# Kernel tuning notes

Hardware: AMD Instinct MI355X
Metric: run time of the kernel (lower is better)

## Reference

```python
import jax, jax.numpy as jnp
import numpy as np

N_NODES = 50000
N_EDGES = 1600000
IN_DIM = 6
H = 64


def _sage_conv(x, src, dst, W_l, b_l, W_r, num_nodes):
    """PyG SAGEConv (aggr='mean'): out = lin_l(mean_{j in N(i)} x_j) + lin_r(x_i).
    lin_l has bias, lin_r has no bias (PyG default)."""
    # mean-aggregate neighbor features at destination nodes
    agg = jax.ops.segment_sum(x[src], dst, num_segments=num_nodes)          # [N, d]
    cnt = jax.ops.segment_sum(jnp.ones((src.shape[0],), x.dtype), dst,
                              num_segments=num_nodes)                        # [N]
    mean = agg / jnp.maximum(cnt, 1.0)[:, None]
    return mean @ W_l + b_l + x @ W_r


def setup_inputs() -> dict:
    key = jax.random.key(0)
    ks = jax.random.split(key, 8)
    x = jax.random.normal(ks[0], (N_NODES, IN_DIM), dtype=jnp.float32)
    edge_index = jax.random.randint(ks[1], (2, N_EDGES), 0, N_NODES, dtype=jnp.int64)
    # Kaiming-ish scaled params
    def lin(k, fan_in, fan_out):
        return jax.random.normal(k, (fan_in, fan_out), dtype=jnp.float32) / np.sqrt(fan_in)
    return {
        "x": x,
        "edge_index": edge_index,
        "W1_l": lin(ks[2], IN_DIM, H),
        "b1_l": jnp.zeros((H,), jnp.float32),
        "W1_r": lin(ks[3], IN_DIM, H),
        "W2_l": lin(ks[4], H, H),
        "b2_l": jnp.zeros((H,), jnp.float32),
        "W2_r": lin(ks[5], H, H),
    }


def reference(x, edge_index, W1_l, b1_l, W1_r, W2_l, b2_l, W2_r):
    src, dst = edge_index[0], edge_index[1]
    n = x.shape[0]
    z = jax.nn.relu(_sage_conv(x, src, dst, W1_l, b1_l, W1_r, n))  # [N, H]
    z = _sage_conv(z, src, dst, W2_l, b2_l, W2_r, n)               # [N, H]
    return z
```

## Files before the change

kernel.cpp:

```cpp
#include <hip/hip_runtime.h>

#define N_NODES 50000
#define N_EDGES 1600000
#define IN_DIM 6
#define H 64

#define NBUCKET 196
#define NBLK 196
#define EPB 8192
#define BCAP 10240

#define L2PAD 72

__device__ __forceinline__ float bf2f(unsigned short u) {
    return __uint_as_float(((unsigned int)u) << 16);
}
__device__ __forceinline__ unsigned short f2bf(float f) {
    unsigned int u = __float_as_uint(f);
    u += 0x7fffu + ((u >> 16) & 1u);
    return (unsigned short)(u >> 16);
}

__global__ __launch_bounds__(256) void scatter_bucketed(
        const int* __restrict__ ei,
        int* __restrict__ gcur,
        unsigned int* __restrict__ ebin,
        const float* __restrict__ W2l,
        const float* __restrict__ W2r,
        unsigned short* __restrict__ Wlt,
        unsigned short* __restrict__ Wrt) {
    int t = threadIdx.x;
    if (blockIdx.x == NBLK) {
        for (int i = t; i < H * H; i += 256) {
            int k = i >> 6, f = i & 63;
            Wlt[f * H + k] = f2bf(W2l[i]);
            Wrt[f * H + k] = f2bf(W2r[i]);
        }
        return;
    }
    __shared__ unsigned int sedge[EPB];
    __shared__ int hist[NBUCKET];
    __shared__ int cur[NBUCKET];
    for (int i = t; i < NBUCKET; i += 256) hist[i] = 0;
    __syncthreads();
    int e0 = blockIdx.x * EPB;
    int cnt = min(EPB, N_EDGES - e0);
    const int4* s4 = (const int4*)(ei + e0);
    const int4* d4 = (const int4*)(ei + N_EDGES + e0);
    for (int k = t; k * 4 < cnt; k += 256) {
        int4 sv = s4[k];
        int4 dv = d4[k];
        sedge[k * 4 + 0] = ((unsigned)sv.x << 16) | (unsigned)dv.x;
        sedge[k * 4 + 1] = ((unsigned)sv.y << 16) | (unsigned)dv.y;
        sedge[k * 4 + 2] = ((unsigned)sv.z << 16) | (unsigned)dv.z;
        sedge[k * 4 + 3] = ((unsigned)sv.w << 16) | (unsigned)dv.w;
        atomicAdd(&hist[dv.x >> 8], 1);
        atomicAdd(&hist[dv.y >> 8], 1);
        atomicAdd(&hist[dv.z >> 8], 1);
        atomicAdd(&hist[dv.w >> 8], 1);
    }
    __syncthreads();
    for (int i = t; i < NBUCKET; i += 256)
        cur[i] = atomicAdd(&gcur[i], hist[i]);
    __syncthreads();
    for (int k = t; k * 4 < cnt; k += 256) {
#pragma unroll
        for (int j = 0; j < 4; j++) {
            unsigned int p = sedge[k * 4 + j];
            int b = (int)(p & 0xffffu) >> 8;
            int pos = atomicAdd(&cur[b], 1);
            if (pos < BCAP) ebin[b * BCAP + pos] = p;
        }
    }
}

__global__ __launch_bounds__(256) void bucket_build(
        const unsigned int* __restrict__ ebin,
        const int* __restrict__ gcur,
        int2* __restrict__ rowpair,
        unsigned short* __restrict__ esrc) {
    __shared__ int raw[BCAP];
    __shared__ unsigned short ssrc[BCAP];
    __shared__ int sdeg[256];
    __shared__ int scur[256];
    __shared__ int wsum[4];
    int t = threadIdx.x, lane = t & 63, w = t >> 6;
    int b = blockIdx.x;
    int base = b << 8;
    int nn = min(256, N_NODES - base);
    int ebase = b * BCAP;
    int cnt = min(gcur[b], BCAP);

    sdeg[t] = 0;
    for (int i = t; i < cnt; i += 256) raw[i] = (int)ebin[ebase + i];
    __syncthreads();
    for (int i = t; i < cnt; i += 256) atomicAdd(&sdeg[raw[i] & 0xff], 1);
    __syncthreads();
    int v = sdeg[t], s = v;
#pragma unroll
    for (int off = 1; off < 64; off <<= 1) {
        int u = __shfl_up(s, off);
        if (lane >= off) s += u;
    }
    if (lane == 63) wsum[w] = s;
    __syncthreads();
    int woff2 = 0;
    for (int k = 0; k < w; k++) woff2 += wsum[k];
    int excl = s - v + woff2;
    if (t < nn) rowpair[base + t] = make_int2(ebase + excl, ebase + excl + v);
    scur[t] = excl;
    __syncthreads();
    for (int i = t; i < cnt; i += 256) {
        int p = raw[i];
        int pos = atomicAdd(&scur[p & 0xff], 1);
        ssrc[pos] = (unsigned short)(((unsigned)p) >> 16);
    }
    __syncthreads();
    for (int i = t; i < cnt; i += 256)
        esrc[ebase + i] = ssrc[i];
}

__global__ __launch_bounds__(256) void layer1_fused(
        const float* __restrict__ x,
        const int2* __restrict__ rowpair,
        const unsigned short* __restrict__ esrc,
        const float* __restrict__ W1l,
        const float* __restrict__ b1,
        const float* __restrict__ W1r,
        unsigned short* __restrict__ z) {
    __shared__ float sWl[IN_DIM * H];
    __shared__ float sWr[IN_DIM * H];
    int t = threadIdx.x;
    for (int i = t; i < IN_DIM * H; i += 256) {
        sWl[i] = W1l[i];
        sWr[i] = W1r[i];
    }
    __syncthreads();

    int wid = t >> 6, lane = t & 63;
    int n = blockIdx.x * 4 + wid;
    if (n >= N_NODES) {
        if (t < H) z[(size_t)N_NODES * H + t] = 0;
        return;
    }
    int2 rp = rowpair[n];
    int r0 = rp.x, r1 = rp.y;
    int nh = 2 * (r1 - r0);
    int half = lane & 1;
    float a0 = 0.f, a1 = 0.f, a2 = 0.f;
    for (int hh = lane; hh < nh; hh += 64) {
        int src = esrc[r0 + (hh >> 1)];
        const float* xs = x + (size_t)src * IN_DIM + half * 3;
        a0 += xs[0]; a1 += xs[1]; a2 += xs[2];
    }
#pragma unroll
    for (int off = 2; off < 64; off <<= 1) {
        a0 += __shfl_xor(a0, off);
        a1 += __shfl_xor(a1, off);
        a2 += __shfl_xor(a2, off);
    }
    float m[IN_DIM];
    m[0] = __shfl(a0, 0); m[1] = __shfl(a1, 0); m[2] = __shfl(a2, 0);
    m[3] = __shfl(a0, 1); m[4] = __shfl(a1, 1); m[5] = __shfl(a2, 1);
    float inv = 1.0f / fmaxf((float)(r1 - r0), 1.0f);

    const float* xn = x + (size_t)n * IN_DIM;
    float acc = b1[lane];
#pragma unroll
    for (int k = 0; k < IN_DIM; k++) {
        acc += m[k] * inv * sWl[k * H + lane] + xn[k] * sWr[k * H + lane];
    }
    z[(size_t)n * H + lane] = f2bf(fmaxf(acc, 0.0f));
}

__global__ __launch_bounds__(256) void layer2_mfma(
        const unsigned short* __restrict__ zin,
        const int2* __restrict__ rowpair,
        const unsigned short* __restrict__ esrc,
        const unsigned short* __restrict__ Wlt,
        const float* __restrict__ b2,
        const unsigned short* __restrict__ Wrt,
        float* __restrict__ out) {
    typedef short bf16x8 __attribute__((ext_vector_type(8)));
    typedef float f32x4 __attribute__((ext_vector_type(4)));
    __shared__ __attribute__((aligned(16))) unsigned short smean[16 * L2PAD];
    __shared__ __attribute__((aligned(16))) unsigned short szl[16 * L2PAD];
    __shared__ __attribute__((aligned(16))) unsigned short sWl[64 * L2PAD];
    __shared__ __attribute__((aligned(16))) unsigned short sWr[64 * L2PAD];

    int t = threadIdx.x;
    int w = t >> 6, lane = t & 63;
    int g = lane >> 4, lg = lane & 15;
    int n0 = blockIdx.x * 16;

    {
        const ushort4* wl4 = (const ushort4*)Wlt;
        const ushort4* wr4 = (const ushort4*)Wrt;
        for (int qi = t; qi < H * H / 4; qi += 256) {
            int f = qi >> 4, kq = qi & 15;
            *(ushort4*)&sWl[f * L2PAD + kq * 4] = wl4[qi];
            *(ushort4*)&sWr[f * L2PAD + kq * 4] = wr4[qi];
        }
    }

    for (int q = 0; q < 4; q++) {
        int ln = w * 4 + q;
        int n = n0 + ln;
        int2 rp = rowpair[n];
        int r0 = rp.x, r1 = rp.y;
        float4 acc = make_float4(0.f, 0.f, 0.f, 0.f);
        for (int base = r0; base < r1; base += 64) {
            int ii = base + lane;
            int idx = (ii < r1) ? (int)esrc[ii] : N_NODES;
            int rem = r1 - base;
#pragma unroll 1
            for (int c = 0; c < 64; c += 16) {
                if (c >= rem) break;
#pragma unroll
                for (int tt = 0; tt < 4; tt++) {
                    int j = c + tt * 4 + g;
                    int s = __shfl(idx, j);
                    const ushort4* zr = (const ushort4*)(zin + (size_t)s * H);
                    ushort4 v = zr[lg];
                    acc.x += bf2f(v.x); acc.y += bf2f(v.y);
                    acc.z += bf2f(v.z); acc.w += bf2f(v.w);
                }
            }
        }
#pragma unroll
        for (int off = 16; off < 64; off <<= 1) {
            acc.x += __shfl_xor(acc.x, off);
            acc.y += __shfl_xor(acc.y, off);
            acc.z += __shfl_xor(acc.z, off);
            acc.w += __shfl_xor(acc.w, off);
        }
        float inv = 1.0f / fmaxf((float)(r1 - r0), 1.0f);
        if (g == 0) {
            ushort4 mb;
            mb.x = f2bf(acc.x * inv); mb.y = f2bf(acc.y * inv);
            mb.z = f2bf(acc.z * inv); mb.w = f2bf(acc.w * inv);
            *(ushort4*)&smean[ln * L2PAD + lg * 4] = mb;
        }
        szl[ln * L2PAD + lane] = zin[(size_t)n * H + lane];
    }
    __syncthreads();

    f32x4 acc = {0.f, 0.f, 0.f, 0.f};
#pragma unroll
    for (int ks = 0; ks < 2; ks++) {
        int ko = ks * 32 + g * 8;
        bf16x8 aM = *(const bf16x8*)&smean[lg * L2PAD + ko];
        bf16x8 aZ = *(const bf16x8*)&szl[lg * L2PAD + ko];
        bf16x8 bL = *(const bf16x8*)&sWl[(w * 16 + lg) * L2PAD + ko];
        bf16x8 bR = *(const bf16x8*)&sWr[(w * 16 + lg) * L2PAD + ko];
        acc = __builtin_amdgcn_mfma_f32_16x16x32_bf16(aM, bL, acc, 0, 0, 0);
        acc = __builtin_amdgcn_mfma_f32_16x16x32_bf16(aZ, bR, acc, 0, 0, 0);
    }
    float bias = b2[w * 16 + lg];
#pragma unroll
    for (int r = 0; r < 4; r++) {
        int node = n0 + g * 4 + r;
        out[(size_t)node * H + w * 16 + lg] = acc[r] + bias;
    }
}

extern "C" void kernel_launch(void* const* d_in, const int* in_sizes, int n_in,
                              void* d_out, int out_size, void* d_ws, size_t ws_size,
                              hipStream_t stream) {
    const float* x   = (const float*)d_in[0];
    const int*   ei  = (const int*)d_in[1];
    const float* W1l = (const float*)d_in[2];
    const float* b1  = (const float*)d_in[3];
    const float* W1r = (const float*)d_in[4];
    const float* W2l = (const float*)d_in[5];
    const float* b2  = (const float*)d_in[6];
    const float* W2r = (const float*)d_in[7];
    float* out = (float*)d_out;

    int* gcur = (int*)d_ws;
    int2* rowpair = (int2*)(gcur + 208);
    unsigned int*   ebin = (unsigned int*)(rowpair + N_NODES);
    unsigned short* esrc = (unsigned short*)(ebin + NBUCKET * BCAP);
    unsigned short* z    = esrc + NBUCKET * BCAP;
    unsigned short* Wlt  = z + (size_t)(N_NODES + 1) * H;
    unsigned short* Wrt  = Wlt + H * H;

    hipMemsetAsync(gcur, 0, NBUCKET * sizeof(int), stream);

    scatter_bucketed<<<NBLK + 1, 256, 0, stream>>>(ei, gcur, ebin,
                                                   W2l, W2r, Wlt, Wrt);
    bucket_build<<<NBUCKET, 256, 0, stream>>>(ebin, gcur, rowpair, esrc);

    layer1_fused<<<N_NODES / 4 + 1, 256, 0, stream>>>(x, rowpair, esrc,
                                                      W1l, b1, W1r, z);
    layer2_mfma<<<N_NODES / 16, 256, 0, stream>>>(z, rowpair, esrc,
                                                  Wlt, b2, Wrt, out);
}
```

Baseline: 161.8 us.

## Fuse CSR bucket build with layer-1 aggregation and linear in one kernel

Merges bucket_build and layer1_fused into one 512-thread kernel per 256-node bucket. Each block now reads neighbour indices from shared memory, gathers x with two threads per node, stores the means in LDS and computes the 6->64 linear layer there. This removes one kernel launch and the global round trip of esrc and rowpair before layer 1. Bucket capacity is cut to 9216, which saves memory and shared space but risks dropping edges if a bucket overflows. Layer 1 now runs on only 196 blocks, which lowers parallelism for the gather.

```diff
diff --git a/kernel.cpp b/kernel.cpp
--- a/kernel.cpp
+++ b/kernel.cpp
@@ -8,7 +8,7 @@
 #define NBUCKET 196
 #define NBLK 196
 #define EPB 8192
-#define BCAP 10240
+#define BCAP 9216
 
 #define L2PAD 72
 
@@ -28,7 +28,8 @@
         const float* __restrict__ W2l,
         const float* __restrict__ W2r,
         unsigned short* __restrict__ Wlt,
-        unsigned short* __restrict__ Wrt) {
+        unsigned short* __restrict__ Wrt,
+        unsigned short* __restrict__ z) {
     int t = threadIdx.x;
     if (blockIdx.x == NBLK) {
         for (int i = t; i < H * H; i += 256) {
@@ -36,6 +37,7 @@
             Wlt[f * H + k] = f2bf(W2l[i]);
             Wrt[f * H + k] = f2bf(W2r[i]);
         }
+        if (t < H) z[(size_t)N_NODES * H + t] = 0;
         return;
     }
     __shared__ unsigned int sedge[EPB];
@@ -69,108 +71,122 @@
             unsigned int p = sedge[k * 4 + j];
             int b = (int)(p & 0xffffu) >> 8;
             int pos = atomicAdd(&cur[b], 1);
-            if (pos < BCAP) ebin[b * BCAP + pos] = p;
-        }
-    }
-}
-
-__global__ __launch_bounds__(256) void bucket_build(
+            if (pos < BCAP) ebin[(size_t)b * BCAP + pos] = p;
+        }
+    }
+}
+
+__global__ __launch_bounds__(512) void bucket_layer1(
         const unsigned int* __restrict__ ebin,
         const int* __restrict__ gcur,
+        const float* __restrict__ x,
+        const float* __restrict__ W1l,
+        const float* __restrict__ b1,
+        const float* __restrict__ W1r,
         int2* __restrict__ rowpair,
-        unsigned short* __restrict__ esrc) {
+        unsigned short* __restrict__ esrc,
+        unsigned short* __restrict__ z) {
     __shared__ int raw[BCAP];
     __shared__ unsigned short ssrc[BCAP];
     __shared__ int sdeg[256];
+    __shared__ int sstart[256];
     __shared__ int scur[256];
     __shared__ int wsum[4];
-    int t = threadIdx.x, lane = t & 63, w = t >> 6;
+    __shared__ float sW1l[IN_DIM * H];
+    __shared__ float sW1r[IN_DIM * H];
+    float* smx   = (float*)raw;
+    float* spart = (float*)raw + 4096;
+
+    int t = threadIdx.x;
+    int lane = t & 63, w = t >> 6;
     int b = blockIdx.x;
     int base = b << 8;
     int nn = min(256, N_NODES - base);
     int ebase = b * BCAP;
     int cnt = min(gcur[b], BCAP);
 
-    sdeg[t] = 0;
-    for (int i = t; i < cnt; i += 256) raw[i] = (int)ebin[ebase + i];
-    __syncthreads();
-    for (int i = t; i < cnt; i += 256) atomicAdd(&sdeg[raw[i] & 0xff], 1);
-    __syncthreads();
-    int v = sdeg[t], s = v;
-#pragma unroll
-    for (int off = 1; off < 64; off <<= 1) {
-        int u = __shfl_up(s, off);
-        if (lane >= off) s += u;
-    }
-    if (lane == 63) wsum[w] = s;
-    __syncthreads();
-    int woff2 = 0;
-    for (int k = 0; k < w; k++) woff2 += wsum[k];
-    int excl = s - v + woff2;
-    if (t < nn) rowpair[base + t] = make_int2(ebase + excl, ebase + excl + v);
-    scur[t] = excl;
-    __syncthreads();
-    for (int i = t; i < cnt; i += 256) {
+    if (t < 256) sdeg[t] = 0;
+    for (int i = t; i < IN_DIM * H; i += 512) { sW1l[i] = W1l[i]; sW1r[i] = W1r[i]; }
+    for (int i = t; i < cnt; i += 512) raw[i] = (int)ebin[ebase + i];
+    __syncthreads();
+    for (int i = t; i < cnt; i += 512) atomicAdd(&sdeg[raw[i] & 0xff], 1);
+    __syncthreads();
+    int v = 0, s = 0;
+    if (t < 256) {
+        v = sdeg[t]; s = v;
+#pragma unroll
+        for (int off = 1; off < 64; off <<= 1) {
+            int u = __shfl_up(s, off);
+            if (lane >= off) s += u;
+        }
+        if (lane == 63) wsum[w] = s;
+    }
+    __syncthreads();
+    if (t < 256) {
+        int woff = 0;
+        for (int k = 0; k < w; k++) woff += wsum[k];
+        int excl = s - v + woff;
+        sstart[t] = excl;
+        scur[t] = excl;
+        if (t < nn) rowpair[base + t] = make_int2(ebase + excl, ebase + excl + v);
+    }
+    __syncthreads();
+    for (int i = t; i < cnt; i += 512) {
         int p = raw[i];
         int pos = atomicAdd(&scur[p & 0xff], 1);
-        ssrc[pos] = (unsigned short)(((unsigned)p) >> 16);
-    }
-    __syncthreads();
-    for (int i = t; i < cnt; i += 256)
+        ssrc[pos] = (unsigned short)((unsigned)p >> 16);
+    }
+    __syncthreads();
+    for (int i = t; i < cnt; i += 512)
         esrc[ebase + i] = ssrc[i];
-}
-
-__global__ __launch_bounds__(256) void layer1_fused(
-        const float* __restrict__ x,
-        const int2* __restrict__ rowpair,
-        const unsigned short* __restrict__ esrc,
-        const float* __restrict__ W1l,
-        const float* __restrict__ b1,
-        const float* __restrict__ W1r,
-        unsigned short* __restrict__ z) {
-    __shared__ float sWl[IN_DIM * H];
-    __shared__ float sWr[IN_DIM * H];
-    int t = threadIdx.x;
-    for (int i = t; i < IN_DIM * H; i += 256) {
-        sWl[i] = W1l[i];
-        sWr[i] = W1r[i];
-    }
-    __syncthreads();
-
-    int wid = t >> 6, lane = t & 63;
-    int n = blockIdx.x * 4 + wid;
-    if (n >= N_NODES) {
-        if (t < H) z[(size_t)N_NODES * H + t] = 0;
-        return;
-    }
-    int2 rp = rowpair[n];
-    int r0 = rp.x, r1 = rp.y;
-    int nh = 2 * (r1 - r0);
-    int half = lane & 1;
-    float a0 = 0.f, a1 = 0.f, a2 = 0.f;
-    for (int hh = lane; hh < nh; hh += 64) {
-        int src = esrc[r0 + (hh >> 1)];
-        const float* xs = x + (size_t)src * IN_DIM + half * 3;
-        a0 += xs[0]; a1 += xs[1]; a2 += xs[2];
-    }
-#pragma unroll
-    for (int off = 2; off < 64; off <<= 1) {
-        a0 += __shfl_xor(a0, off);
-        a1 += __shfl_xor(a1, off);
-        a2 += __shfl_xor(a2, off);
-    }
-    float m[IN_DIM];
-    m[0] = __shfl(a0, 0); m[1] = __shfl(a1, 0); m[2] = __shfl(a2, 0);
-    m[3] = __shfl(a0, 1); m[4] = __shfl(a1, 1); m[5] = __shfl(a2, 1);
-    float inv = 1.0f / fmaxf((float)(r1 - r0), 1.0f);
-
-    const float* xn = x + (size_t)n * IN_DIM;
-    float acc = b1[lane];
-#pragma unroll
-    for (int k = 0; k < IN_DIM; k++) {
-        acc += m[k] * inv * sWl[k * H + lane] + xn[k] * sWr[k * H + lane];
-    }
-    z[(size_t)n * H + lane] = f2bf(fmaxf(acc, 0.0f));
+    for (int i = t; i < nn * IN_DIM; i += 512) {
+        int node = i / 6, k = i - node * 6;
+        smx[node * 16 + 6 + k] = x[(size_t)base * IN_DIM + i];
+    }
+
+    int node = t & 255, half = t >> 8;
+    float a0 = 0.f, a1 = 0.f, a2 = 0.f, a3 = 0.f, a4 = 0.f, a5 = 0.f;
+    int deg = 0, st = 0;
+    if (node < nn) { deg = sdeg[node]; st = sstart[node]; }
+    for (int i = st + half; i < st + deg; i += 2) {
+        int src = ssrc[i];
+        const float2* xs = (const float2*)(x + (size_t)src * IN_DIM);
+        float2 p0 = xs[0], p1 = xs[1], p2 = xs[2];
+        a0 += p0.x; a1 += p0.y; a2 += p1.x;
+        a3 += p1.y; a4 += p2.x; a5 += p2.y;
+    }
+    if (half == 1 && node < nn) {
+        spart[node * 6 + 0] = a0; spart[node * 6 + 1] = a1;
+        spart[node * 6 + 2] = a2; spart[node * 6 + 3] = a3;
+        spart[node * 6 + 4] = a4; spart[node * 6 + 5] = a5;
+    }
+    __syncthreads();
+    if (half == 0 && node < nn) {
+        float inv = 1.0f / fmaxf((float)deg, 1.0f);
+        smx[node * 16 + 0] = (a0 + spart[node * 6 + 0]) * inv;
+        smx[node * 16 + 1] = (a1 + spart[node * 6 + 1]) * inv;
+        smx[node * 16 + 2] = (a2 + spart[node * 6 + 2]) * inv;
+        smx[node * 16 + 3] = (a3 + spart[node * 6 + 3]) * inv;
+        smx[node * 16 + 4] = (a4 + spart[node * 6 + 4]) * inv;
+        smx[node * 16 + 5] = (a5 + spart[node * 6 + 5]) * inv;
+    }
+    __syncthreads();
+
+    int feat = t & 63, ng = t >> 6;
+    float wl[IN_DIM], wr[IN_DIM];
+#pragma unroll
+    for (int k = 0; k < IN_DIM; k++) { wl[k] = sW1l[k * H + feat]; wr[k] = sW1r[k * H + feat]; }
+    float bias = b1[feat];
+    for (int nb = ng; nb < nn; nb += 8) {
+        const float4* row = (const float4*)&smx[nb * 16];
+        float4 r0 = row[0], r1 = row[1], r2 = row[2];
+        float acc = bias;
+        acc += r0.x * wl[0] + r0.y * wl[1] + r0.z * wl[2]
+             + r0.w * wl[3] + r1.x * wl[4] + r1.y * wl[5];
+        acc += r1.z * wr[0] + r1.w * wr[1] + r2.x * wr[2]
+             + r2.y * wr[3] + r2.z * wr[4] + r2.w * wr[5];
+        z[(size_t)(base + nb) * H + feat] = f2bf(fmaxf(acc, 0.0f));
+    }
 }
 
 __global__ __launch_bounds__(256) void layer2_mfma(
@@ -221,9 +237,9 @@
                     int j = c + tt * 4 + g;
                     int s = __shfl(idx, j);
                     const ushort4* zr = (const ushort4*)(zin + (size_t)s * H);
-                    ushort4 v = zr[lg];
-                    acc.x += bf2f(v.x); acc.y += bf2f(v.y);
-                    acc.z += bf2f(v.z); acc.w += bf2f(v.w);
+                    ushort4 vv = zr[lg];
+                    acc.x += bf2f(vv.x); acc.y += bf2f(vv.y);
+                    acc.z += bf2f(vv.z); acc.w += bf2f(vv.w);
                 }
             }
         }
@@ -280,19 +296,17 @@
     int* gcur = (int*)d_ws;
     int2* rowpair = (int2*)(gcur + 208);
     unsigned int*   ebin = (unsigned int*)(rowpair + N_NODES);
-    unsigned short* esrc = (unsigned short*)(ebin + NBUCKET * BCAP);
-    unsigned short* z    = esrc + NBUCKET * BCAP;
+    unsigned short* esrc = (unsigned short*)(ebin + (size_t)NBUCKET * BCAP);
+    unsigned short* z    = esrc + (size_t)NBUCKET * BCAP;
     unsigned short* Wlt  = z + (size_t)(N_NODES + 1) * H;
     unsigned short* Wrt  = Wlt + H * H;
 
     hipMemsetAsync(gcur, 0, NBUCKET * sizeof(int), stream);
 
     scatter_bucketed<<<NBLK + 1, 256, 0, stream>>>(ei, gcur, ebin,
-                                                   W2l, W2r, Wlt, Wrt);
-    bucket_build<<<NBUCKET, 256, 0, stream>>>(ebin, gcur, rowpair, esrc);
-
-    layer1_fused<<<N_NODES / 4 + 1, 256, 0, stream>>>(x, rowpair, esrc,
-                                                      W1l, b1, W1r, z);
+                                                   W2l, W2r, Wlt, Wrt, z);
+    bucket_layer1<<<NBUCKET, 512, 0, stream>>>(ebin, gcur, x, W1l, b1, W1r,
+                                               rowpair, esrc, z);
     layer2_mfma<<<N_NODES / 16, 256, 0, stream>>>(z, rowpair, esrc,
                                                   Wlt, b2, Wrt, out);
 }
```

Result: faster. 152.2 us (-5.9%).
